# Optimization experiments

Hardware: AMD Instinct MI355X
Metric: run time of the kernel (lower is better)

The kernel has to match this reference:

```python
import jax, jax.numpy as jnp
import numpy as np

L, B, S, D = 12, 4, 1024, 1024
EPS = 1e-5  # torch LayerNorm default


def setup_inputs() -> dict:
    key = jax.random.key(0)
    k1, k2, k3 = jax.random.split(key, 3)
    return {
        "layer_history": jax.random.normal(k1, (L, B, S, D), jnp.float32),
        "current": jax.random.normal(k2, (B, S, D), jnp.float32),
        "w": jax.random.normal(k3, (D,), jnp.float32) * (1.0 / D ** 0.5),
        "gamma": jnp.ones((D,), jnp.float32),
        "beta": jnp.zeros((D,), jnp.float32),
    }


def reference(layer_history, current, w, gamma, beta):
    # V: [L+1, B, S, D] -- all history layers plus the current layer
    V = jnp.concatenate([layer_history, current[None]], axis=0)
    L1 = V.shape[0]
    Bc, Sc, Dc = current.shape

    # LayerNorm over last dim (biased variance, like torch)
    mu = jnp.mean(V, axis=-1, keepdims=True)
    var = jnp.mean((V - mu) ** 2, axis=-1, keepdims=True)
    K = (V - mu) * jax.lax.rsqrt(var + EPS) * gamma + beta

    # pseudo-query scores: one scalar per (layer, batch, key-pos)
    scores = jnp.einsum('d,lbsd->bls', w, K)  # [B, L1, S]

    # broadcast over query index t, causal mask on key index s (s > t masked)
    causal = jnp.triu(jnp.ones((Sc, Sc), bool), 1)          # [t, s]
    s4 = jnp.where(causal[None, :, None, :], -jnp.inf,
                   scores[:, None, :, :])                   # [B, S, L1, S]

    # softmax jointly over all (layer, key-pos) pairs
    wts = jax.nn.softmax(s4.reshape(Bc, Sc, L1 * Sc), axis=-1)
    wts = wts.reshape(Bc, Sc, L1, Sc)

    # weighted sum over values (V un-normalized)
    h = jnp.einsum('btls,lbsd->btd', wts, V)  # [B, S, D]
    return h
```

## Files before the change

### kernel.cpp

```cpp
#include <hip/hip_runtime.h>
#include <math.h>

namespace {
constexpr int L1 = 13;
constexpr int LH = 12;
constexpr int B  = 4;
constexpr int S  = 1024;
constexpr int D  = 1024;
constexpr int NCH  = 32;
constexpr int CH   = S / NCH;
constexpr int DBLK = D / 256;

constexpr int OFF_Z    = 0;
constexpr int OFF_ZCUM = B * S;
constexpr int OFF_CS   = 2 * B * S;
constexpr float EPS = 1e-5f;

typedef float float4n __attribute__((ext_vector_type(4)));

__device__ __forceinline__ float4n ntload4(const float* p) {
    return __builtin_nontemporal_load((const float4n*)p);
}
}

__global__ __launch_bounds__(256) void arm_k1(const float* __restrict__ hist,
                                              const float* __restrict__ cur,
                                              const float* __restrict__ w,
                                              const float* __restrict__ gamma,
                                              const float* __restrict__ beta,
                                              float* __restrict__ U,
                                              float* __restrict__ ws) {
    const int tid = threadIdx.x, lane = tid & 63;
    const int gw = blockIdx.x * 4 + (tid >> 6);
    const int d0 = lane * 4;
    const size_t rowoff = (size_t)gw * D;

    float4n wg[4];
    float swg_p = 0.f, swb_p = 0.f;
#pragma unroll
    for (int j = 0; j < 4; j++) {
        int d = d0 + j * 256;
        float4 wv = *(const float4*)(w + d);
        float4 gv = *(const float4*)(gamma + d);
        float4 bv = *(const float4*)(beta + d);
        wg[j] = (float4n){wv.x * gv.x, wv.y * gv.y, wv.z * gv.z, wv.w * gv.w};
        swg_p += wg[j].x + wg[j].y + wg[j].z + wg[j].w;
        swb_p += wv.x * bv.x + wv.y * bv.y + wv.z * bv.z + wv.w * bv.w;
    }
#pragma unroll
    for (int o = 32; o > 0; o >>= 1) {
        swg_p += __shfl_xor(swg_p, o);
        swb_p += __shfl_xor(swb_p, o);
    }
    const float swg = swg_p, swb = swb_p;

    float4n acc[4] = {{0,0,0,0},{0,0,0,0},{0,0,0,0},{0,0,0,0}};
    float z = 0.f;

#pragma unroll 4
    for (int l = 0; l < L1; l++) {
        const float* row = (l < LH ? hist + (size_t)l * (B * S * D) : cur) + rowoff;
        float4n v[4];
#pragma unroll
        for (int j = 0; j < 4; j++) v[j] = ntload4(row + d0 + j * 256);

        float s1 = 0.f, s2 = 0.f, sw = 0.f;
#pragma unroll
        for (int j = 0; j < 4; j++) {
            s1 += v[j].x + v[j].y + v[j].z + v[j].w;
            s2 += v[j].x * v[j].x + v[j].y * v[j].y + v[j].z * v[j].z + v[j].w * v[j].w;
            sw += wg[j].x * v[j].x + wg[j].y * v[j].y + wg[j].z * v[j].z + wg[j].w * v[j].w;
        }
#pragma unroll
        for (int o = 32; o > 0; o >>= 1) {
            s1 += __shfl_xor(s1, o);
            s2 += __shfl_xor(s2, o);
            sw += __shfl_xor(sw, o);
        }
        float mu   = s1 * (1.0f / D);
        float var  = s2 * (1.0f / D) - mu * mu;
        float rstd = rsqrtf(var + EPS);
        float p = __expf(rstd * (sw - mu * swg) + swb);
#pragma unroll
        for (int j = 0; j < 4; j++) {
            acc[j].x += p * v[j].x; acc[j].y += p * v[j].y;
            acc[j].z += p * v[j].z; acc[j].w += p * v[j].w;
        }
        z += p;
    }

#pragma unroll
    for (int j = 0; j < 4; j++)
        *(float4n*)(U + rowoff + d0 + j * 256) = acc[j];
    if (lane == 0) ws[OFF_Z + gw] = z;
}

__global__ void arm_k2(const float* __restrict__ U, float* __restrict__ ws) {
    int blk = blockIdx.x;
    int tid = threadIdx.x;
    if (blk >= B * NCH * DBLK) {
        int b = blk - B * NCH * DBLK;
        const float* z = ws + OFF_Z + b * S;
        float* zc = ws + OFF_ZCUM + b * S;
        float v[4];
        float loc = 0.f;
#pragma unroll
        for (int j = 0; j < 4; j++) { v[j] = z[tid * 4 + j]; loc += v[j]; }
        __shared__ float lds[256];
        lds[tid] = loc; __syncthreads();
        for (int off = 1; off < 256; off <<= 1) {
            float t = (tid >= off) ? lds[tid - off] : 0.f;
            __syncthreads();
            lds[tid] += t;
            __syncthreads();
        }
        float run = lds[tid] - loc;
#pragma unroll
        for (int j = 0; j < 4; j++) { run += v[j]; zc[tid * 4 + j] = run; }
        return;
    }
    int dblk = blk % DBLK;
    int rem = blk / DBLK;
    int ch = rem % NCH, b = rem / NCH;
    int d = dblk * 256 + tid;
    const float* Ub = U + ((size_t)b * S + ch * CH) * D + d;
    float sum = 0.f;
#pragma unroll
    for (int j = 0; j < CH; j++) sum += Ub[(size_t)j * D];
    ws[OFF_CS + (b * NCH + ch) * D + d] = sum;
}

__global__ void arm_k3(float* __restrict__ U, const float* __restrict__ ws) {
    int blk = blockIdx.x;
    int dblk = blk % DBLK;
    int rem = blk / DBLK;
    int ch = rem % NCH, b = rem / NCH;
    int d = dblk * 256 + threadIdx.x;

    const float* cs = ws + OFF_CS + b * NCH * D + d;
    float run = 0.f;
    for (int c2 = 0; c2 < ch; c2++) run += cs[(size_t)c2 * D];

    const float* zc = ws + OFF_ZCUM + b * S + ch * CH;
    float* Ub = U + ((size_t)b * S + ch * CH) * D + d;
#pragma unroll
    for (int j = 0; j < CH; j++) {
        run += Ub[(size_t)j * D];
        float h = run / zc[j];
        __builtin_nontemporal_store(h, &Ub[(size_t)j * D]);
    }
}

extern "C" void kernel_launch(void* const* d_in, const int* in_sizes, int n_in,
                              void* d_out, int out_size, void* d_ws, size_t ws_size,
                              hipStream_t stream) {
    const float* hist  = (const float*)d_in[0];
    const float* cur   = (const float*)d_in[1];
    const float* w     = (const float*)d_in[2];
    const float* gamma = (const float*)d_in[3];
    const float* beta  = (const float*)d_in[4];
    float* out = (float*)d_out;
    float* ws  = (float*)d_ws;

    arm_k1<<<B * S / 4, 256, 0, stream>>>(hist, cur, w, gamma, beta, out, ws);
    arm_k2<<<B * NCH * DBLK + B, 256, 0, stream>>>(out, ws);
    arm_k3<<<B * NCH * DBLK, 256, 0, stream>>>(out, ws);
}
```

Measured before the change: 66.84 us.

## Fuse chunk partial sums into row kernel and drop nontemporal hints

```diff
diff --git a/kernel.cpp b/kernel.cpp
--- a/kernel.cpp
+++ b/kernel.cpp
@@ -10,17 +10,16 @@
 constexpr int NCH  = 32;
 constexpr int CH   = S / NCH;
 constexpr int DBLK = D / 256;
+constexpr int RPB  = 8;
+constexpr int NPS  = B * S / RPB;
 
 constexpr int OFF_Z    = 0;
 constexpr int OFF_ZCUM = B * S;
 constexpr int OFF_CS   = 2 * B * S;
+constexpr int OFF_PS   = OFF_CS + B * NCH * D;
 constexpr float EPS = 1e-5f;
 
 typedef float float4n __attribute__((ext_vector_type(4)));
-
-__device__ __forceinline__ float4n ntload4(const float* p) {
-    return __builtin_nontemporal_load((const float4n*)p);
-}
 }
 
 __global__ __launch_bounds__(256) void arm_k1(const float* __restrict__ hist,
@@ -30,22 +29,25 @@
                                               const float* __restrict__ beta,
                                               float* __restrict__ U,
                                               float* __restrict__ ws) {
-    const int tid = threadIdx.x, lane = tid & 63;
-    const int gw = blockIdx.x * 4 + (tid >> 6);
+    const int tid = threadIdx.x, lane = tid & 63, wid = tid >> 6;
+    const int blk = blockIdx.x;
+    const int row0 = blk * RPB + wid * 2;
     const int d0 = lane * 4;
-    const size_t rowoff = (size_t)gw * D;
+
+    __shared__ float cs[4][D];
 
     float4n wg[4];
     float swg_p = 0.f, swb_p = 0.f;
 #pragma unroll
     for (int j = 0; j < 4; j++) {
         int d = d0 + j * 256;
-        float4 wv = *(const float4*)(w + d);
-        float4 gv = *(const float4*)(gamma + d);
-        float4 bv = *(const float4*)(beta + d);
-        wg[j] = (float4n){wv.x * gv.x, wv.y * gv.y, wv.z * gv.z, wv.w * gv.w};
+        float4n wv = *(const float4n*)(w + d);
+        float4n gv = *(const float4n*)(gamma + d);
+        float4n bv = *(const float4n*)(beta + d);
+        wg[j] = wv * gv;
         swg_p += wg[j].x + wg[j].y + wg[j].z + wg[j].w;
-        swb_p += wv.x * bv.x + wv.y * bv.y + wv.z * bv.z + wv.w * bv.w;
+        float4n wb = wv * bv;
+        swb_p += wb.x + wb.y + wb.z + wb.w;
     }
 #pragma unroll
     for (int o = 32; o > 0; o >>= 1) {
@@ -54,52 +56,73 @@
     }
     const float swg = swg_p, swb = swb_p;
 
-    float4n acc[4] = {{0,0,0,0},{0,0,0,0},{0,0,0,0},{0,0,0,0}};
-    float z = 0.f;
+#pragma unroll
+    for (int r = 0; r < 2; r++) {
+        const size_t rowoff = (size_t)(row0 + r) * D;
+        float4n acc[4] = {{0,0,0,0},{0,0,0,0},{0,0,0,0},{0,0,0,0}};
+        float z = 0.f;
 
-#pragma unroll 4
-    for (int l = 0; l < L1; l++) {
-        const float* row = (l < LH ? hist + (size_t)l * (B * S * D) : cur) + rowoff;
-        float4n v[4];
+#pragma unroll 2
+        for (int l = 0; l < L1; l++) {
+            const float* row = (l < LH ? hist + (size_t)l * (B * S * D) : cur) + rowoff;
+            float4n v[4];
 #pragma unroll
-        for (int j = 0; j < 4; j++) v[j] = ntload4(row + d0 + j * 256);
+            for (int j = 0; j < 4; j++) v[j] = *(const float4n*)(row + d0 + j * 256);
 
-        float s1 = 0.f, s2 = 0.f, sw = 0.f;
+            float s1 = 0.f, s2 = 0.f, sw = 0.f;
 #pragma unroll
-        for (int j = 0; j < 4; j++) {
-            s1 += v[j].x + v[j].y + v[j].z + v[j].w;
-            s2 += v[j].x * v[j].x + v[j].y * v[j].y + v[j].z * v[j].z + v[j].w * v[j].w;
-            sw += wg[j].x * v[j].x + wg[j].y * v[j].y + wg[j].z * v[j].z + wg[j].w * v[j].w;
+            for (int j = 0; j < 4; j++) {
+                s1 += v[j].x + v[j].y + v[j].z + v[j].w;
+                s2 += v[j].x * v[j].x + v[j].y * v[j].y + v[j].z * v[j].z + v[j].w * v[j].w;
+                sw += wg[j].x * v[j].x + wg[j].y * v[j].y + wg[j].z * v[j].z + wg[j].w * v[j].w;
+            }
+#pragma unroll
+            for (int o = 32; o > 0; o >>= 1) {
+                s1 += __shfl_xor(s1, o);
+                s2 += __shfl_xor(s2, o);
+                sw += __shfl_xor(sw, o);
+            }
+            float mu   = s1 * (1.0f / D);
+            float var  = s2 * (1.0f / D) - mu * mu;
+            float rstd = rsqrtf(var + EPS);
+            float p = __expf(rstd * (sw - mu * swg) + swb);
+#pragma unroll
+            for (int j = 0; j < 4; j++) acc[j] += v[j] * p;
+            z += p;
         }
+
 #pragma unroll
-        for (int o = 32; o > 0; o >>= 1) {
-            s1 += __shfl_xor(s1, o);
-            s2 += __shfl_xor(s2, o);
-            sw += __shfl_xor(sw, o);
+        for (int j = 0; j < 4; j++)
+            *(float4n*)(U + rowoff + d0 + j * 256) = acc[j];
+        if (lane == 0) ws[OFF_Z + row0 + r] = z;
+
+        if (r == 0) {
+#pragma unroll
+            for (int j = 0; j < 4; j++)
+                *(float4n*)&cs[wid][d0 + j * 256] = acc[j];
+        } else {
+#pragma unroll
+            for (int j = 0; j < 4; j++) {
+                float4n t = *(float4n*)&cs[wid][d0 + j * 256];
+                *(float4n*)&cs[wid][d0 + j * 256] = t + acc[j];
+            }
         }
-        float mu   = s1 * (1.0f / D);
-        float var  = s2 * (1.0f / D) - mu * mu;
-        float rstd = rsqrtf(var + EPS);
-        float p = __expf(rstd * (sw - mu * swg) + swb);
-#pragma unroll
-        for (int j = 0; j < 4; j++) {
-            acc[j].x += p * v[j].x; acc[j].y += p * v[j].y;
-            acc[j].z += p * v[j].z; acc[j].w += p * v[j].w;
-        }
-        z += p;
     }
 
-#pragma unroll
-    for (int j = 0; j < 4; j++)
-        *(float4n*)(U + rowoff + d0 + j * 256) = acc[j];
-    if (lane == 0) ws[OFF_Z + gw] = z;
+    __syncthreads();
+    const int c = tid * 4;
+    float4n ps = *(float4n*)&cs[0][c];
+    ps += *(float4n*)&cs[1][c];
+    ps += *(float4n*)&cs[2][c];
+    ps += *(float4n*)&cs[3][c];
+    *(float4n*)(ws + OFF_PS + (size_t)blk * D + c) = ps;
 }
 
-__global__ void arm_k2(const float* __restrict__ U, float* __restrict__ ws) {
+__global__ void arm_k2(float* __restrict__ ws) {
     int blk = blockIdx.x;
     int tid = threadIdx.x;
-    if (blk >= B * NCH * DBLK) {
-        int b = blk - B * NCH * DBLK;
+    if (blk >= B * NCH) {
+        int b = blk - B * NCH;
         const float* z = ws + OFF_Z + b * S;
         float* zc = ws + OFF_ZCUM + b * S;
         float v[4];
@@ -119,15 +142,13 @@
         for (int j = 0; j < 4; j++) { run += v[j]; zc[tid * 4 + j] = run; }
         return;
     }
-    int dblk = blk % DBLK;
-    int rem = blk / DBLK;
-    int ch = rem % NCH, b = rem / NCH;
-    int d = dblk * 256 + tid;
-    const float* Ub = U + ((size_t)b * S + ch * CH) * D + d;
-    float sum = 0.f;
+    int b = blk / NCH, ch = blk % NCH;
+    int c = tid * 4;
+    float4n s = {0, 0, 0, 0};
 #pragma unroll
-    for (int j = 0; j < CH; j++) sum += Ub[(size_t)j * D];
-    ws[OFF_CS + (b * NCH + ch) * D + d] = sum;
+    for (int k = 0; k < 4; k++)
+        s += *(const float4n*)(ws + OFF_PS + (size_t)((b * S / RPB) + ch * 4 + k) * D + c);
+    *(float4n*)(ws + OFF_CS + (size_t)blk * D + c) = s;
 }
 
 __global__ void arm_k3(float* __restrict__ U, const float* __restrict__ ws) {
@@ -146,8 +167,7 @@
 #pragma unroll
     for (int j = 0; j < CH; j++) {
         run += Ub[(size_t)j * D];
-        float h = run / zc[j];
-        __builtin_nontemporal_store(h, &Ub[(size_t)j * D]);
+        Ub[(size_t)j * D] = run / zc[j];
     }
 }
 
@@ -162,7 +182,7 @@
     float* out = (float*)d_out;
     float* ws  = (float*)d_ws;
 
-    arm_k1<<<B * S / 4, 256, 0, stream>>>(hist, cur, w, gamma, beta, out, ws);
-    arm_k2<<<B * NCH * DBLK + B, 256, 0, stream>>>(out, ws);
+    arm_k1<<<B * S / RPB, 256, 0, stream>>>(hist, cur, w, gamma, beta, out, ws);
+    arm_k2<<<B * NCH + B, 256, 0, stream>>>(ws);
     arm_k3<<<B * NCH * DBLK, 256, 0, stream>>>(out, ws);
 }
```

Result: faster. 60.59 us (-9.3%).
